# Performance work log

Hardware: AMD Instinct MI355X
Metric: run time of the kernel (lower is better)

## Reference

```python
import jax, jax.numpy as jnp
import numpy as np

B, S, H = 2, 2048, 1024
NH, HD = 16, 64  # num heads, head dim
EPS = 1e-12

def layernorm(x, g, b):
    mu = jnp.mean(x, axis=-1, keepdims=True)
    var = jnp.mean(jnp.square(x - mu), axis=-1, keepdims=True)
    return (x - mu) / jnp.sqrt(var + EPS) * g + b

def setup_inputs() -> dict:
    key = jax.random.key(0)
    ks = jax.random.split(key, 6)
    sd = 0.02
    return {
        "x": jax.random.normal(ks[0], (B, S, H), jnp.float32),
        "ln1_g": jnp.ones((H,), jnp.float32),
        "ln1_b": jnp.zeros((H,), jnp.float32),
        "w_qkv": jax.random.normal(ks[1], (H, 3 * H), jnp.float32) * sd,
        "b_qkv": jnp.zeros((3 * H,), jnp.float32),
        "w_dense": jax.random.normal(ks[2], (H, H), jnp.float32) * sd,
        "b_dense": jnp.zeros((H,), jnp.float32),
        "ln2_g": jnp.ones((H,), jnp.float32),
        "ln2_b": jnp.zeros((H,), jnp.float32),
        "w_fc1": jax.random.normal(ks[3], (H, 2 * H), jnp.float32) * sd,
        "w_fc2": jax.random.normal(ks[4], (2 * H, H), jnp.float32) * sd,
        "b_fc2": jnp.zeros((H,), jnp.float32),
    }

def reference(x, ln1_g, ln1_b, w_qkv, b_qkv, w_dense, b_dense,
              ln2_g, ln2_b, w_fc1, w_fc2, b_fc2):
    b, s, h = x.shape
    qkv = layernorm(x, ln1_g, ln1_b) @ w_qkv + b_qkv          # (b, s, 3h)
    q, k, v = jnp.split(qkv, 3, axis=-1)
    # (b, s, h) -> (b, nh, s, hd)
    reshape = lambda t: t.reshape(b, s, NH, HD).transpose(0, 2, 1, 3)
    q, k, v = reshape(q), reshape(k), reshape(v)
    scores = jnp.einsum('bhqd,bhkd->bhqk', q, k) / jnp.sqrt(jnp.float32(HD))
    causal = jnp.tril(jnp.ones((s, s), dtype=bool))
    scores = jnp.where(causal, scores, -jnp.inf)
    probs = jax.nn.softmax(scores, axis=-1)
    attn = jnp.einsum('bhqk,bhkd->bhqd', probs, v)            # (b, nh, s, hd)
    attn = attn.transpose(0, 2, 1, 3).reshape(b, s, h)
    out = x + (attn @ w_dense + b_dense)
    m = layernorm(out, ln2_g, ln2_b)
    mlp = jax.nn.gelu(m @ w_fc1, approximate=False) @ w_fc2 + b_fc2
    return out + mlp
```

## Files before the change

### kernel.cpp

```cpp
#include <hip/hip_runtime.h>
#include <hip/hip_bf16.h>

typedef __bf16 bf16x8 __attribute__((ext_vector_type(8)));
typedef float  f32x4  __attribute__((ext_vector_type(4)));

typedef __attribute__((address_space(3))) unsigned int as3_u32;
typedef __attribute__((address_space(1))) unsigned int as1_u32;

__device__ __forceinline__ void gld_lds16(const void* gptr, void* lptr){
  __builtin_amdgcn_global_load_lds((const as1_u32*)gptr, (as3_u32*)lptr, 16, 0, 0);
}

__global__ __launch_bounds__(256) void transpose_all(
    const float* __restrict__ w_qkv, const float* __restrict__ w_dense,
    const float* __restrict__ w_fc1, const float* __restrict__ w_fc2,
    __bf16* __restrict__ oqkv, __bf16* __restrict__ oden,
    __bf16* __restrict__ ofc1, __bf16* __restrict__ ofc2){
  __shared__ float tile[32][33];
  int idx = blockIdx.x;
  const float* in; __bf16* out; int R, C;
  if (idx < 3072){ in = w_qkv;  out = oqkv; R = 1024; C = 3072; }
  else if (idx < 4096){ idx -= 3072; in = w_dense; out = oden; R = 1024; C = 1024; }
  else if (idx < 6144){ idx -= 4096; in = w_fc1;  out = ofc1; R = 1024; C = 2048; }
  else { idx -= 6144; in = w_fc2;  out = ofc2; R = 2048; C = 1024; }
  const int ntx = C >> 5;
  const int c0 = (idx % ntx)*32, r0 = (idx / ntx)*32;
  const int tx = threadIdx.x, ty = threadIdx.y;
  #pragma unroll
  for (int i=0;i<32;i+=8)
    tile[ty+i][tx] = in[(size_t)(r0+ty+i)*C + c0+tx];
  __syncthreads();
  #pragma unroll
  for (int i=0;i<32;i+=8)
    out[(size_t)(c0+ty+i)*R + r0+tx] = (__bf16)tile[tx][ty+i];
}

__global__ __launch_bounds__(256) void ln_kernel(const float* __restrict__ x, const float* __restrict__ g,
                                                 const float* __restrict__ b, __bf16* __restrict__ out){
  const int row = blockIdx.x, t = threadIdx.x;
  const float4 v = ((const float4*)(x + (size_t)row*1024))[t];
  float s = v.x+v.y+v.z+v.w;
  #pragma unroll
  for (int m=1;m<64;m<<=1) s += __shfl_xor(s, m);
  __shared__ float red[8];
  if ((t&63)==0) red[t>>6] = s;
  __syncthreads();
  const float mu = (red[0]+red[1]+red[2]+red[3]) * (1.f/1024.f);
  const float d0=v.x-mu, d1=v.y-mu, d2=v.z-mu, d3=v.w-mu;
  float sq = d0*d0+d1*d1+d2*d2+d3*d3;
  #pragma unroll
  for (int m=1;m<64;m<<=1) sq += __shfl_xor(sq, m);
  if ((t&63)==0) red[4+(t>>6)] = sq;
  __syncthreads();
  const float var = (red[4]+red[5]+red[6]+red[7]) * (1.f/1024.f);
  const float inv = rsqrtf(var + 1e-12f);
  const float4 gv = ((const float4*)g)[t];
  const float4 bv = ((const float4*)b)[t];
  union { __bf16 h[4]; uint2 u; } pk;
  pk.h[0]=(__bf16)(d0*inv*gv.x+bv.x); pk.h[1]=(__bf16)(d1*inv*gv.y+bv.y);
  pk.h[2]=(__bf16)(d2*inv*gv.z+bv.z); pk.h[3]=(__bf16)(d3*inv*gv.w+bv.w);
  *(uint2*)(out + (size_t)row*1024 + t*4) = pk.u;
}

template<int MODE>
__global__ __launch_bounds__(256) void gemm_bt(
    const __bf16* __restrict__ A, const __bf16* __restrict__ Bt,
    const float* __restrict__ bias,
    __bf16* __restrict__ outB,
    __bf16* __restrict__ qO, __bf16* __restrict__ kO, __bf16* __restrict__ vtO,
    int M, int N, int K)
{
  __shared__ __align__(16) __bf16 As[2][128*32];
  __shared__ __align__(16) __bf16 Bs[2][128*32];
  const int tid = threadIdx.x;
  const int lane = tid & 63, wave = tid >> 6;
  const int wr = wave >> 1, wc = wave & 1;
  const int l15 = lane & 15, lg = lane >> 4;
  const int bm = blockIdx.x, bn = blockIdx.y;
  const __bf16* Ab = A  + (size_t)bm*128*K;
  const __bf16* Bb = Bt + (size_t)bn*128*K;
  f32x4 acc[4][4] = {};
  const int r0 = tid >> 2;
  const int c0 = (tid & 3) * 8;

  auto stage = [&](int kt, int b){
    const int k0 = kt*32;
    char* dA = (char*)&As[b][0] + wave*1024;
    char* dB = (char*)&Bs[b][0] + wave*1024;
    gld_lds16(Ab + (size_t)r0*K      + k0 + c0, dA);
    gld_lds16(Ab + (size_t)(r0+64)*K + k0 + c0, dA + 4096);
    gld_lds16(Bb + (size_t)r0*K      + k0 + c0, dB);
    gld_lds16(Bb + (size_t)(r0+64)*K + k0 + c0, dB + 4096);
  };

  const int nk = K >> 5;
  stage(0, 0);
  __syncthreads();
  for (int kt = 0; kt < nk; ++kt){
    const int b = kt & 1;
    if (kt+1 < nk) stage(kt+1, b^1);
    bf16x8 af[4], bfv[4];
    #pragma unroll
    for (int i=0;i<4;++i){
      af[i]  = *(const bf16x8*)&As[b][(wr*64 + i*16 + l15)*32 + lg*8];
      bfv[i] = *(const bf16x8*)&Bs[b][(wc*64 + i*16 + l15)*32 + lg*8];
    }
    #pragma unroll
    for (int i=0;i<4;++i)
      #pragma unroll
      for (int j=0;j<4;++j)
        acc[i][j] = __builtin_amdgcn_mfma_f32_16x16x32_bf16(af[i], bfv[j], acc[i][j], 0,0,0);
    __syncthreads();
  }
  #pragma unroll
  for (int i=0;i<4;++i){
    #pragma unroll
    for (int j=0;j<4;++j){
      const int col = bn*128 + wc*64 + j*16 + l15;
      float bv;
      if constexpr (MODE==2) bv = 0.f; else bv = bias[col];
      #pragma unroll
      for (int r=0;r<4;++r){
        const int row = bm*128 + wr*64 + i*16 + lg*4 + r;
        float v = acc[i][j][r] + bv;
        if constexpr (MODE==0){
          const int b_ = row >> 11, s_ = row & 2047;
          if (col < 1024){
            const int h = col>>6, d = col&63;
            qO[((size_t)(b_*16+h)*2048 + s_)*64 + d] = (__bf16)v;
          } else if (col < 2048){
            const int h = (col-1024)>>6, d = (col-1024)&63;
            kO[((size_t)(b_*16+h)*2048 + s_)*64 + d] = (__bf16)v;
          } else {
            const int h = (col-2048)>>6, d = (col-2048)&63;
            vtO[((size_t)(b_*16+h)*64 + d)*2048 + s_] = (__bf16)v;
          }
        } else {
          const float gl = 0.5f*v*(1.f + erff(v*0.70710678118f));
          outB[(size_t)row*N + col] = (__bf16)gl;
        }
      }
    }
  }
}

__global__ __launch_bounds__(256) void gemm_bt64(
    const __bf16* __restrict__ A, const __bf16* __restrict__ Bt,
    const float* __restrict__ bias, const float* __restrict__ resid,
    float* __restrict__ outF, int M, int N, int K)
{
  __shared__ __align__(16) __bf16 As[2][128*32];
  __shared__ __align__(16) __bf16 Bs[2][64*32];
  const int tid = threadIdx.x;
  const int lane = tid & 63, wave = tid >> 6;
  const int l15 = lane & 15, lg = lane >> 4;
  const int bm = blockIdx.x, bn = blockIdx.y;
  const __bf16* Ab = A  + (size_t)bm*128*K;
  const __bf16* Bb = Bt + (size_t)bn*64*K;
  f32x4 acc[2][4] = {};
  const int r0 = tid >> 2;
  const int c0 = (tid & 3) * 8;

  auto stage = [&](int kt, int b){
    const int k0 = kt*32;
    char* dA = (char*)&As[b][0] + wave*1024;
    char* dB = (char*)&Bs[b][0] + wave*1024;
    gld_lds16(Ab + (size_t)r0*K      + k0 + c0, dA);
    gld_lds16(Ab + (size_t)(r0+64)*K + k0 + c0, dA + 4096);
    gld_lds16(Bb + (size_t)r0*K      + k0 + c0, dB);
  };

  const int nk = K >> 5;
  stage(0, 0);
  __syncthreads();
  for (int kt = 0; kt < nk; ++kt){
    const int b = kt & 1;
    if (kt+1 < nk) stage(kt+1, b^1);
    bf16x8 af[2], bfv[4];
    #pragma unroll
    for (int i=0;i<2;++i)
      af[i]  = *(const bf16x8*)&As[b][(wave*32 + i*16 + l15)*32 + lg*8];
    #pragma unroll
    for (int j=0;j<4;++j)
      bfv[j] = *(const bf16x8*)&Bs[b][(j*16 + l15)*32 + lg*8];
    #pragma unroll
    for (int i=0;i<2;++i)
      #pragma unroll
      for (int j=0;j<4;++j)
        acc[i][j] = __builtin_amdgcn_mfma_f32_16x16x32_bf16(af[i], bfv[j], acc[i][j], 0,0,0);
    __syncthreads();
  }
  #pragma unroll
  for (int i=0;i<2;++i){
    #pragma unroll
    for (int j=0;j<4;++j){
      const int col = bn*64 + j*16 + l15;
      const float bv = bias[col];
      #pragma unroll
      for (int r=0;r<4;++r){
        const int row = bm*128 + wave*32 + i*16 + lg*4 + r;
        outF[(size_t)row*N + col] = acc[i][j][r] + bv + resid[(size_t)row*N + col];
      }
    }
  }
}

__global__ __launch_bounds__(512, 4) void attn_kernel(
    const __bf16* __restrict__ Q, const __bf16* __restrict__ K,
    const __bf16* __restrict__ Vt, __bf16* __restrict__ out)
{
  __shared__ __align__(16) __bf16 Ks[2][128*64];
  __shared__ __align__(16) __bf16 Vs[2][2][64*64];
  __shared__ __align__(16) __bf16 Pl[8][16*64];
  const int tid = threadIdx.x;
  const int lane = tid & 63, wave = tid >> 6;
  const int l15 = lane & 15, lg = lane >> 4;
  const int bh = blockIdx.y;
  const int nqb = (int)gridDim.x;
  const int qblk = (bh & 16) ? (int)blockIdx.x : (nqb - 1 - (int)blockIdx.x);
  const int qb = qblk * 128;
  const int qw = qb + wave*16;
  const __bf16* Qh = Q + (size_t)bh*2048*64;
  const char*  Khc = (const char*)(K  + (size_t)bh*2048*64);
  const char*  Vhc = (const char*)(Vt + (size_t)bh*64*2048);

  bf16x8 qf[2];
  #pragma unroll
  for (int f=0;f<2;++f){
    bf16x8 t8 = *(const bf16x8*)&Qh[(size_t)(qw + l15)*64 + f*32 + lg*8];
    #pragma unroll
    for (int j=0;j<8;++j) t8[j] = (__bf16)((float)t8[j] * 0.125f);
    qf[f] = t8;
  }

  f32x4 oacc[4] = {};
  float mrun = -1e30f, lrun = 0.f;

  const int swz_st = (((lane&7) ^ (lane>>3)) << 4);
  const int rswz = ((l15 & 7) << 4);
  char* Pw = (char*)&Pl[wave][0];

  const int krow = wave*16 + (lane>>3);
  const int kh   = wave & 1;
  const int dgrp = wave >> 1;
  const int vrow = dgrp*16 + (lane>>3);

  const int nst = qblk + 1;

  {
    gld_lds16(Khc + (size_t)krow*128 + swz_st,     (char*)&Ks[0][0] + wave*2048);
    gld_lds16(Khc + (size_t)(krow+8)*128 + swz_st, (char*)&Ks[0][0] + wave*2048 + 1024);
    const char* s = Vhc + kh*128 + swz_st;
    gld_lds16(s + (size_t)vrow*4096,     (char*)&Vs[0][kh][0] + dgrp*2048);
    gld_lds16(s + (size_t)(vrow+8)*4096, (char*)&Vs[0][kh][0] + dgrp*2048 + 1024);
  }
  __syncthreads();

  for (int st = 0; st < nst; ++st){
    const int cur = st & 1;
    const int kv0 = st*128;
    if (st+1 < nst){
      const size_t nkv0 = (size_t)(kv0 + 128);
      gld_lds16(Khc + (nkv0 + krow)*128 + swz_st,     (char*)&Ks[cur^1][0] + wave*2048);
      gld_lds16(Khc + (nkv0 + krow + 8)*128 + swz_st, (char*)&Ks[cur^1][0] + wave*2048 + 1024);
      const char* s = Vhc + nkv0*2 + kh*128 + swz_st;
      gld_lds16(s + (size_t)vrow*4096,     (char*)&Vs[cur^1][kh][0] + dgrp*2048);
      gld_lds16(s + (size_t)(vrow+8)*4096, (char*)&Vs[cur^1][kh][0] + dgrp*2048 + 1024);
    }
    if (kv0 <= qw + 15){
      const char* Kb = (const char*)&Ks[cur][0];
      f32x4 sc[8];
      #pragma unroll
      for (int t=0;t<8;++t) sc[t] = f32x4{0.f,0.f,0.f,0.f};
      #pragma unroll
      for (int t=0;t<8;++t){
        const int row = t*16 + l15;
        bf16x8 k0 = *(const bf16x8*)(Kb + row*128 + ((lg*16)      ^ rswz));
        bf16x8 k1 = *(const bf16x8*)(Kb + row*128 + ((64 + lg*16) ^ rswz));
        sc[t] = __builtin_amdgcn_mfma_f32_16x16x32_bf16(k0, qf[0], sc[t], 0,0,0);
        sc[t] = __builtin_amdgcn_mfma_f32_16x16x32_bf16(k1, qf[1], sc[t], 0,0,0);
      }
      if (kv0 + 127 > qw){
        const int q = qw + l15;
        #pragma unroll
        for (int t=0;t<8;++t)
          #pragma unroll
          for (int r=0;r<4;++r)
            if (kv0 + t*16 + lg*4 + r > q) sc[t][r] = -1e30f;
      }
      f32x4 mm;
      #pragma unroll
      for (int r=0;r<4;++r){
        float a = fmaxf(fmaxf(sc[0][r],sc[1][r]), fmaxf(sc[2][r],sc[3][r]));
        float b = fmaxf(fmaxf(sc[4][r],sc[5][r]), fmaxf(sc[6][r],sc[7][r]));
        mm[r] = fmaxf(a,b);
      }
      float mx = fmaxf(fmaxf(mm[0],mm[1]), fmaxf(mm[2],mm[3]));
      mx = fmaxf(mx, __shfl_xor(mx, 16));
      mx = fmaxf(mx, __shfl_xor(mx, 32));
      if (!__all(mx <= mrun + 8.0f)){
        const float nm = fmaxf(mrun, mx);
        const float co = exp2f((mrun - nm) * 1.44269504f);
        lrun *= co;
        float cor[4];
        #pragma unroll
        for (int r=0;r<4;++r) cor[r] = __shfl(co, lg*4+r);
        #pragma unroll
        for (int c=0;c<4;++c)
          #pragma unroll
          for (int r=0;r<4;++r)
            oacc[c][r] *= cor[r];
        mrun = nm;
      }
      const float mb = mrun * 1.44269504f;
      #pragma unroll
      for (int t=0;t<8;++t)
        #pragma unroll
        for (int r=0;r<4;++r)
          sc[t][r] = exp2f(sc[t][r]*1.44269504f - mb);
      f32x4 ss;
      #pragma unroll
      for (int r=0;r<4;++r){
        float a = (sc[0][r]+sc[1][r]) + (sc[2][r]+sc[3][r]);
        float b = (sc[4][r]+sc[5][r]) + (sc[6][r]+sc[7][r]);
        ss[r] = a + b;
      }
      float rs = (ss[0]+ss[1]) + (ss[2]+ss[3]);
      rs += __shfl_xor(rs, 16);
      rs += __shfl_xor(rs, 32);
      lrun += rs;
      #pragma unroll
      for (int h=0; h<2; ++h){
        #pragma unroll
        for (int t=0;t<4;++t){
          union { __bf16 hh[4]; uint2 u; } pk4;
          pk4.hh[0] = (__bf16)sc[h*4+t][0];
          pk4.hh[1] = (__bf16)sc[h*4+t][1];
          pk4.hh[2] = (__bf16)sc[h*4+t][2];
          pk4.hh[3] = (__bf16)sc[h*4+t][3];
          *(uint2*)(Pw + l15*128 + ((t*32 + lg*8) ^ rswz)) = pk4.u;
        }
        const char* Vb = (const char*)&Vs[cur][h][0];
        #pragma unroll
        for (int f=0;f<2;++f){
          bf16x8 pa = *(const bf16x8*)(Pw + l15*128 + ((f*64 + lg*16) ^ rswz));
          #pragma unroll
          for (int c=0;c<4;++c){
            bf16x8 vf = *(const bf16x8*)(Vb + (c*16+l15)*128 + ((f*64 + lg*16) ^ rswz));
            oacc[c] = __builtin_amdgcn_mfma_f32_16x16x32_bf16(pa, vf, oacc[c], 0,0,0);
          }
        }
      }
    }
    __syncthreads();
  }

  const int b_ = bh >> 4, h_ = bh & 15;
  float lr[4];
  #pragma unroll
  for (int r=0;r<4;++r) lr[r] = __shfl(lrun, lg*4+r);
  #pragma unroll
  for (int c=0;c<4;++c)
    #pragma unroll
    for (int r=0;r<4;++r){
      const int row = qw + lg*4 + r;
      out[((size_t)(b_*2048 + row))*1024 + h_*64 + c*16 + l15] = (__bf16)(oacc[c][r] / lr[r]);
    }
}

extern "C" void kernel_launch(void* const* d_in, const int* in_sizes, int n_in,
                              void* d_out, int out_size, void* d_ws, size_t ws_size,
                              hipStream_t stream) {
  const float* x      = (const float*)d_in[0];
  const float* ln1_g  = (const float*)d_in[1];
  const float* ln1_b  = (const float*)d_in[2];
  const float* w_qkv  = (const float*)d_in[3];
  const float* b_qkv  = (const float*)d_in[4];
  const float* w_dense= (const float*)d_in[5];
  const float* b_dense= (const float*)d_in[6];
  const float* ln2_g  = (const float*)d_in[7];
  const float* ln2_b  = (const float*)d_in[8];
  const float* w_fc1  = (const float*)d_in[9];
  const float* w_fc2  = (const float*)d_in[10];
  const float* b_fc2  = (const float*)d_in[11];

  char* ws = (char*)d_ws;
  __bf16* wqkvT  = (__bf16*)(ws + 0);
  __bf16* wdenT  = (__bf16*)(ws + 6291456);
  __bf16* wfc1T  = (__bf16*)(ws + 8388608);
  __bf16* wfc2T  = (__bf16*)(ws + 12582912);
  __bf16* xn     = (__bf16*)(ws + 16777216);
  __bf16* Qb     = (__bf16*)(ws + 25165824);
  __bf16* Kb     = (__bf16*)(ws + 33554432);
  __bf16* Vtb    = (__bf16*)(ws + 41943040);
  __bf16* attnb  = (__bf16*)(ws + 50331648);
  float*  outf   = (float*) (ws + 58720256);
  __bf16* mb     = (__bf16*)(ws + 75497472);
  __bf16* h1b    = (__bf16*)(ws + 83886080);

  transpose_all<<<8192, dim3(32,8), 0, stream>>>(w_qkv, w_dense, w_fc1, w_fc2,
                                                 wqkvT, wdenT, wfc1T, wfc2T);
  ln_kernel<<<4096, 256, 0, stream>>>(x, ln1_g, ln1_b, xn);
  gemm_bt<0><<<dim3(32,24), 256, 0, stream>>>(xn, wqkvT, b_qkv,
                                              nullptr, Qb, Kb, Vtb, 4096, 3072, 1024);
  attn_kernel<<<dim3(16,32), 512, 0, stream>>>(Qb, Kb, Vtb, attnb);
  gemm_bt64<<<dim3(32,16), 256, 0, stream>>>(attnb, wdenT, b_dense, x,
                                             outf, 4096, 1024, 1024);
  ln_kernel<<<4096, 256, 0, stream>>>(outf, ln2_g, ln2_b, mb);
  gemm_bt<2><<<dim3(32,16), 256, 0, stream>>>(mb, wfc1T, nullptr,
                                              h1b, nullptr, nullptr, nullptr, 4096, 2048, 1024);
  gemm_bt64<<<dim3(32,16), 256, 0, stream>>>(h1b, wfc2T, b_fc2, outf,
                                             (float*)d_out, 4096, 1024, 2048);
}
```

Baseline: 192.4 us.

## Process 32 query rows per wave in attention, halving waves per block

The attention kernel now runs 4 waves per block instead of 8. Each wave handles two 16-row query tiles, so every K and V fragment read from LDS feeds two MFMAs instead of one. This is meant to cut LDS read traffic and per-wave softmax overhead for each unit of MFMA work. In exchange it raises register pressure (two sets of scores and accumulators), lowers occupancy, and drops the per-wave causal skip of fully masked tiles, which adds wasted compute on diagonal blocks.

```diff
diff --git a/kernel.cpp b/kernel.cpp
--- a/kernel.cpp
+++ b/kernel.cpp
@@ -205,13 +205,13 @@
   }
 }
 
-__global__ __launch_bounds__(512, 4) void attn_kernel(
+__global__ __launch_bounds__(256, 2) void attn_kernel(
     const __bf16* __restrict__ Q, const __bf16* __restrict__ K,
     const __bf16* __restrict__ Vt, __bf16* __restrict__ out)
 {
   __shared__ __align__(16) __bf16 Ks[2][128*64];
   __shared__ __align__(16) __bf16 Vs[2][2][64*64];
-  __shared__ __align__(16) __bf16 Pl[8][16*64];
+  __shared__ __align__(16) __bf16 Pl[4][32*64];
   const int tid = threadIdx.x;
   const int lane = tid & 63, wave = tid >> 6;
   const int l15 = lane & 15, lg = lane >> 4;
@@ -219,40 +219,41 @@
   const int nqb = (int)gridDim.x;
   const int qblk = (bh & 16) ? (int)blockIdx.x : (nqb - 1 - (int)blockIdx.x);
   const int qb = qblk * 128;
-  const int qw = qb + wave*16;
+  const int qw = qb + wave*32;
   const __bf16* Qh = Q + (size_t)bh*2048*64;
   const char*  Khc = (const char*)(K  + (size_t)bh*2048*64);
   const char*  Vhc = (const char*)(Vt + (size_t)bh*64*2048);
 
-  bf16x8 qf[2];
-  #pragma unroll
-  for (int f=0;f<2;++f){
-    bf16x8 t8 = *(const bf16x8*)&Qh[(size_t)(qw + l15)*64 + f*32 + lg*8];
-    #pragma unroll
-    for (int j=0;j<8;++j) t8[j] = (__bf16)((float)t8[j] * 0.125f);
-    qf[f] = t8;
-  }
-
-  f32x4 oacc[4] = {};
-  float mrun = -1e30f, lrun = 0.f;
+  bf16x8 qf[2][2];
+  #pragma unroll
+  for (int qi=0;qi<2;++qi)
+    #pragma unroll
+    for (int f=0;f<2;++f){
+      bf16x8 t8 = *(const bf16x8*)&Qh[(size_t)(qw + qi*16 + l15)*64 + f*32 + lg*8];
+      #pragma unroll
+      for (int j=0;j<8;++j) t8[j] = (__bf16)((float)t8[j] * 0.125f);
+      qf[qi][f] = t8;
+    }
+
+  f32x4 oacc[2][4] = {};
+  float mrun[2] = {-1e30f, -1e30f}, lrun[2] = {0.f, 0.f};
 
   const int swz_st = (((lane&7) ^ (lane>>3)) << 4);
   const int rswz = ((l15 & 7) << 4);
   char* Pw = (char*)&Pl[wave][0];
 
-  const int krow = wave*16 + (lane>>3);
+  const int krow = wave*32 + (lane>>3);
   const int kh   = wave & 1;
   const int dgrp = wave >> 1;
-  const int vrow = dgrp*16 + (lane>>3);
+  const int vrow = dgrp*32 + (lane>>3);
 
   const int nst = qblk + 1;
 
-  {
-    gld_lds16(Khc + (size_t)krow*128 + swz_st,     (char*)&Ks[0][0] + wave*2048);
-    gld_lds16(Khc + (size_t)(krow+8)*128 + swz_st, (char*)&Ks[0][0] + wave*2048 + 1024);
-    const char* s = Vhc + kh*128 + swz_st;
-    gld_lds16(s + (size_t)vrow*4096,     (char*)&Vs[0][kh][0] + dgrp*2048);
-    gld_lds16(s + (size_t)(vrow+8)*4096, (char*)&Vs[0][kh][0] + dgrp*2048 + 1024);
+  #pragma unroll
+  for (int i=0;i<4;++i){
+    gld_lds16(Khc + (size_t)(krow + i*8)*128 + swz_st, (char*)&Ks[0][0] + wave*4096 + i*1024);
+    gld_lds16(Vhc + (size_t)(vrow + i*8)*4096 + kh*128 + swz_st,
+              (char*)&Vs[0][kh][0] + dgrp*4096 + i*1024);
   }
   __syncthreads();
 
@@ -261,93 +262,119 @@
     const int kv0 = st*128;
     if (st+1 < nst){
       const size_t nkv0 = (size_t)(kv0 + 128);
-      gld_lds16(Khc + (nkv0 + krow)*128 + swz_st,     (char*)&Ks[cur^1][0] + wave*2048);
-      gld_lds16(Khc + (nkv0 + krow + 8)*128 + swz_st, (char*)&Ks[cur^1][0] + wave*2048 + 1024);
-      const char* s = Vhc + nkv0*2 + kh*128 + swz_st;
-      gld_lds16(s + (size_t)vrow*4096,     (char*)&Vs[cur^1][kh][0] + dgrp*2048);
-      gld_lds16(s + (size_t)(vrow+8)*4096, (char*)&Vs[cur^1][kh][0] + dgrp*2048 + 1024);
-    }
-    if (kv0 <= qw + 15){
+      #pragma unroll
+      for (int i=0;i<4;++i){
+        gld_lds16(Khc + (nkv0 + krow + i*8)*128 + swz_st,
+                  (char*)&Ks[cur^1][0] + wave*4096 + i*1024);
+        gld_lds16(Vhc + (size_t)(vrow + i*8)*4096 + nkv0*2 + kh*128 + swz_st,
+                  (char*)&Vs[cur^1][kh][0] + dgrp*4096 + i*1024);
+      }
+    }
+    {
       const char* Kb = (const char*)&Ks[cur][0];
-      f32x4 sc[8];
-      #pragma unroll
-      for (int t=0;t<8;++t) sc[t] = f32x4{0.f,0.f,0.f,0.f};
+      f32x4 sc[2][8];
+      #pragma unroll
+      for (int qi=0;qi<2;++qi)
+        #pragma unroll
+        for (int t=0;t<8;++t) sc[qi][t] = f32x4{0.f,0.f,0.f,0.f};
       #pragma unroll
       for (int t=0;t<8;++t){
         const int row = t*16 + l15;
         bf16x8 k0 = *(const bf16x8*)(Kb + row*128 + ((lg*16)      ^ rswz));
         bf16x8 k1 = *(const bf16x8*)(Kb + row*128 + ((64 + lg*16) ^ rswz));
-        sc[t] = __builtin_amdgcn_mfma_f32_16x16x32_bf16(k0, qf[0], sc[t], 0,0,0);
-        sc[t] = __builtin_amdgcn_mfma_f32_16x16x32_bf16(k1, qf[1], sc[t], 0,0,0);
+        sc[0][t] = __builtin_amdgcn_mfma_f32_16x16x32_bf16(k0, qf[0][0], sc[0][t], 0,0,0);
+        sc[0][t] = __builtin_amdgcn_mfma_f32_16x16x32_bf16(k1, qf[0][1], sc[0][t], 0,0,0);
+        sc[1][t] = __builtin_amdgcn_mfma_f32_16x16x32_bf16(k0, qf[1][0], sc[1][t], 0,0,0);
+        sc[1][t] = __builtin_amdgcn_mfma_f32_16x16x32_bf16(k1, qf[1][1], sc[1][t], 0,0,0);
       }
       if (kv0 + 127 > qw){
-        const int q = qw + l15;
+        #pragma unroll
+        for (int qi=0;qi<2;++qi){
+          const int q = qw + qi*16 + l15;
+          #pragma unroll
+          for (int t=0;t<8;++t)
+            #pragma unroll
+            for (int r=0;r<4;++r)
+              if (kv0 + t*16 + lg*4 + r > q) sc[qi][t][r] = -1e30f;
+        }
+      }
+      float mx[2];
+      #pragma unroll
+      for (int qi=0;qi<2;++qi){
+        f32x4 mm;
+        #pragma unroll
+        for (int r=0;r<4;++r){
+          float a = fmaxf(fmaxf(sc[qi][0][r],sc[qi][1][r]), fmaxf(sc[qi][2][r],sc[qi][3][r]));
+          float b = fmaxf(fmaxf(sc[qi][4][r],sc[qi][5][r]), fmaxf(sc[qi][6][r],sc[qi][7][r]));
+          mm[r] = fmaxf(a,b);
+        }
+        float m = fmaxf(fmaxf(mm[0],mm[1]), fmaxf(mm[2],mm[3]));
+        m = fmaxf(m, __shfl_xor(m, 16));
+        m = fmaxf(m, __shfl_xor(m, 32));
+        mx[qi] = m;
+      }
+      if (!__all((mx[0] <= mrun[0] + 8.0f) && (mx[1] <= mrun[1] + 8.0f))){
+        #pragma unroll
+        for (int qi=0;qi<2;++qi){
+          const float nm = fmaxf(mrun[qi], mx[qi]);
+          const float co = exp2f((mrun[qi] - nm) * 1.44269504f);
+          lrun[qi] *= co;
+          float cor[4];
+          #pragma unroll
+          for (int r=0;r<4;++r) cor[r] = __shfl(co, lg*4+r);
+          #pragma unroll
+          for (int c=0;c<4;++c)
+            #pragma unroll
+            for (int r=0;r<4;++r)
+              oacc[qi][c][r] *= cor[r];
+          mrun[qi] = nm;
+        }
+      }
+      #pragma unroll
+      for (int qi=0;qi<2;++qi){
+        const float mb = mrun[qi] * 1.44269504f;
         #pragma unroll
         for (int t=0;t<8;++t)
           #pragma unroll
           for (int r=0;r<4;++r)
-            if (kv0 + t*16 + lg*4 + r > q) sc[t][r] = -1e30f;
-      }
-      f32x4 mm;
-      #pragma unroll
-      for (int r=0;r<4;++r){
-        float a = fmaxf(fmaxf(sc[0][r],sc[1][r]), fmaxf(sc[2][r],sc[3][r]));
-        float b = fmaxf(fmaxf(sc[4][r],sc[5][r]), fmaxf(sc[6][r],sc[7][r]));
-        mm[r] = fmaxf(a,b);
-      }
-      float mx = fmaxf(fmaxf(mm[0],mm[1]), fmaxf(mm[2],mm[3]));
-      mx = fmaxf(mx, __shfl_xor(mx, 16));
-      mx = fmaxf(mx, __shfl_xor(mx, 32));
-      if (!__all(mx <= mrun + 8.0f)){
-        const float nm = fmaxf(mrun, mx);
-        const float co = exp2f((mrun - nm) * 1.44269504f);
-        lrun *= co;
-        float cor[4];
-        #pragma unroll
-        for (int r=0;r<4;++r) cor[r] = __shfl(co, lg*4+r);
-        #pragma unroll
-        for (int c=0;c<4;++c)
-          #pragma unroll
-          for (int r=0;r<4;++r)
-            oacc[c][r] *= cor[r];
-        mrun = nm;
-      }
-      const float mb = mrun * 1.44269504f;
-      #pragma unroll
-      for (int t=0;t<8;++t)
-        #pragma unroll
-        for (int r=0;r<4;++r)
-          sc[t][r] = exp2f(sc[t][r]*1.44269504f - mb);
-      f32x4 ss;
-      #pragma unroll
-      for (int r=0;r<4;++r){
-        float a = (sc[0][r]+sc[1][r]) + (sc[2][r]+sc[3][r]);
-        float b = (sc[4][r]+sc[5][r]) + (sc[6][r]+sc[7][r]);
-        ss[r] = a + b;
-      }
-      float rs = (ss[0]+ss[1]) + (ss[2]+ss[3]);
-      rs += __shfl_xor(rs, 16);
-      rs += __shfl_xor(rs, 32);
-      lrun += rs;
+            sc[qi][t][r] = exp2f(sc[qi][t][r]*1.44269504f - mb);
+        f32x4 ss;
+        #pragma unroll
+        for (int r=0;r<4;++r){
+          float a = (sc[qi][0][r]+sc[qi][1][r]) + (sc[qi][2][r]+sc[qi][3][r]);
+          float b = (sc[qi][4][r]+sc[qi][5][r]) + (sc[qi][6][r]+sc[qi][7][r]);
+          ss[r] = a + b;
+        }
+        float rs = (ss[0]+ss[1]) + (ss[2]+ss[3]);
+        rs += __shfl_xor(rs, 16);
+        rs += __shfl_xor(rs, 32);
+        lrun[qi] += rs;
+      }
       #pragma unroll
       for (int h=0; h<2; ++h){
         #pragma unroll
-        for (int t=0;t<4;++t){
-          union { __bf16 hh[4]; uint2 u; } pk4;
-          pk4.hh[0] = (__bf16)sc[h*4+t][0];
-          pk4.hh[1] = (__bf16)sc[h*4+t][1];
-          pk4.hh[2] = (__bf16)sc[h*4+t][2];
-          pk4.hh[3] = (__bf16)sc[h*4+t][3];
-          *(uint2*)(Pw + l15*128 + ((t*32 + lg*8) ^ rswz)) = pk4.u;
+        for (int qi=0;qi<2;++qi){
+          char* Pq = Pw + qi*2048;
+          #pragma unroll
+          for (int t=0;t<4;++t){
+            union { __bf16 hh[4]; uint2 u; } pk4;
+            pk4.hh[0] = (__bf16)sc[qi][h*4+t][0];
+            pk4.hh[1] = (__bf16)sc[qi][h*4+t][1];
+            pk4.hh[2] = (__bf16)sc[qi][h*4+t][2];
+            pk4.hh[3] = (__bf16)sc[qi][h*4+t][3];
+            *(uint2*)(Pq + l15*128 + ((t*32 + lg*8) ^ rswz)) = pk4.u;
+          }
         }
         const char* Vb = (const char*)&Vs[cur][h][0];
         #pragma unroll
         for (int f=0;f<2;++f){
-          bf16x8 pa = *(const bf16x8*)(Pw + l15*128 + ((f*64 + lg*16) ^ rswz));
+          bf16x8 pa0 = *(const bf16x8*)(Pw +        l15*128 + ((f*64 + lg*16) ^ rswz));
+          bf16x8 pa1 = *(const bf16x8*)(Pw + 2048 + l15*128 + ((f*64 + lg*16) ^ rswz));
           #pragma unroll
           for (int c=0;c<4;++c){
             bf16x8 vf = *(const bf16x8*)(Vb + (c*16+l15)*128 + ((f*64 + lg*16) ^ rswz));
-            oacc[c] = __builtin_amdgcn_mfma_f32_16x16x32_bf16(pa, vf, oacc[c], 0,0,0);
+            oacc[0][c] = __builtin_amdgcn_mfma_f32_16x16x32_bf16(pa0, vf, oacc[0][c], 0,0,0);
+            oacc[1][c] = __builtin_amdgcn_mfma_f32_16x16x32_bf16(pa1, vf, oacc[1][c], 0,0,0);
           }
         }
       }
@@ -356,16 +383,19 @@
   }
 
   const int b_ = bh >> 4, h_ = bh & 15;
-  float lr[4];
-  #pragma unroll
-  for (int r=0;r<4;++r) lr[r] = __shfl(lrun, lg*4+r);
-  #pragma unroll
-  for (int c=0;c<4;++c)
-    #pragma unroll
-    for (int r=0;r<4;++r){
-      const int row = qw + lg*4 + r;
-      out[((size_t)(b_*2048 + row))*1024 + h_*64 + c*16 + l15] = (__bf16)(oacc[c][r] / lr[r]);
-    }
+  #pragma unroll
+  for (int qi=0;qi<2;++qi){
+    float lr[4];
+    #pragma unroll
+    for (int r=0;r<4;++r) lr[r] = __shfl(lrun[qi], lg*4+r);
+    #pragma unroll
+    for (int c=0;c<4;++c)
+      #pragma unroll
+      for (int r=0;r<4;++r){
+        const int row = qw + qi*16 + lg*4 + r;
+        out[((size_t)(b_*2048 + row))*1024 + h_*64 + c*16 + l15] = (__bf16)(oacc[qi][c][r] / lr[r]);
+      }
+  }
 }
 
 extern "C" void kernel_launch(void* const* d_in, const int* in_sizes, int n_in,
@@ -403,7 +433,7 @@
   ln_kernel<<<4096, 256, 0, stream>>>(x, ln1_g, ln1_b, xn);
   gemm_bt<0><<<dim3(32,24), 256, 0, stream>>>(xn, wqkvT, b_qkv,
                                               nullptr, Qb, Kb, Vtb, 4096, 3072, 1024);
-  attn_kernel<<<dim3(16,32), 512, 0, stream>>>(Qb, Kb, Vtb, attnb);
+  attn_kernel<<<dim3(16,32), 256, 0, stream>>>(Qb, Kb, Vtb, attnb);
   gemm_bt64<<<dim3(32,16), 256, 0, stream>>>(attnb, wdenT, b_dense, x,
                                              outf, 4096, 1024, 1024);
   ln_kernel<<<4096, 256, 0, stream>>>(outf, ln2_g, ln2_b, mb);
```

Measured after the change: 198.2 us. 3.0% more time.

## Fuse weight transpose with first layernorm; stage V-transpose stores through LDS

Applied to the files above, without the earlier changes.

Merges the weight transpose/convert kernel and the first layernorm into one launch, with block index choosing the role. This saves a kernel launch and lets the two independent jobs overlap. In the QKV GEMM epilogue, the V part is written transposed into LDS with an XOR swizzle and then stored as coalesced 16-byte rows, replacing scattered 2-byte strided global writes. This adds extra barriers and LDS traffic in the epilogue.

```diff
diff --git a/kernel.cpp b/kernel.cpp
--- a/kernel.cpp
+++ b/kernel.cpp
@@ -11,28 +11,57 @@
   __builtin_amdgcn_global_load_lds((const as1_u32*)gptr, (as3_u32*)lptr, 16, 0, 0);
 }
 
-__global__ __launch_bounds__(256) void transpose_all(
+__global__ __launch_bounds__(256) void prep_kernel(
     const float* __restrict__ w_qkv, const float* __restrict__ w_dense,
     const float* __restrict__ w_fc1, const float* __restrict__ w_fc2,
     __bf16* __restrict__ oqkv, __bf16* __restrict__ oden,
-    __bf16* __restrict__ ofc1, __bf16* __restrict__ ofc2){
+    __bf16* __restrict__ ofc1, __bf16* __restrict__ ofc2,
+    const float* __restrict__ x, const float* __restrict__ g,
+    const float* __restrict__ b, __bf16* __restrict__ ln_out){
   __shared__ float tile[32][33];
+  const int tid = threadIdx.x;
   int idx = blockIdx.x;
-  const float* in; __bf16* out; int R, C;
-  if (idx < 3072){ in = w_qkv;  out = oqkv; R = 1024; C = 3072; }
-  else if (idx < 4096){ idx -= 3072; in = w_dense; out = oden; R = 1024; C = 1024; }
-  else if (idx < 6144){ idx -= 4096; in = w_fc1;  out = ofc1; R = 1024; C = 2048; }
-  else { idx -= 6144; in = w_fc2;  out = ofc2; R = 2048; C = 1024; }
-  const int ntx = C >> 5;
-  const int c0 = (idx % ntx)*32, r0 = (idx / ntx)*32;
-  const int tx = threadIdx.x, ty = threadIdx.y;
-  #pragma unroll
-  for (int i=0;i<32;i+=8)
-    tile[ty+i][tx] = in[(size_t)(r0+ty+i)*C + c0+tx];
-  __syncthreads();
-  #pragma unroll
-  for (int i=0;i<32;i+=8)
-    out[(size_t)(c0+ty+i)*R + r0+tx] = (__bf16)tile[tx][ty+i];
+  if (idx < 8192){
+    const float* in; __bf16* out; int R, C;
+    if (idx < 3072){ in = w_qkv;  out = oqkv; R = 1024; C = 3072; }
+    else if (idx < 4096){ idx -= 3072; in = w_dense; out = oden; R = 1024; C = 1024; }
+    else if (idx < 6144){ idx -= 4096; in = w_fc1;  out = ofc1; R = 1024; C = 2048; }
+    else { idx -= 6144; in = w_fc2;  out = ofc2; R = 2048; C = 1024; }
+    const int ntx = C >> 5;
+    const int c0 = (idx % ntx)*32, r0 = (idx / ntx)*32;
+    const int tx = tid & 31, ty = tid >> 5;
+    #pragma unroll
+    for (int i=0;i<32;i+=8)
+      tile[ty+i][tx] = in[(size_t)(r0+ty+i)*C + c0+tx];
+    __syncthreads();
+    #pragma unroll
+    for (int i=0;i<32;i+=8)
+      out[(size_t)(c0+ty+i)*R + r0+tx] = (__bf16)tile[tx][ty+i];
+  } else {
+    const int row = idx - 8192;
+    float* red = &tile[0][0];
+    const float4 v = ((const float4*)(x + (size_t)row*1024))[tid];
+    float s = v.x+v.y+v.z+v.w;
+    #pragma unroll
+    for (int m=1;m<64;m<<=1) s += __shfl_xor(s, m);
+    if ((tid&63)==0) red[tid>>6] = s;
+    __syncthreads();
+    const float mu = (red[0]+red[1]+red[2]+red[3]) * (1.f/1024.f);
+    const float d0=v.x-mu, d1=v.y-mu, d2=v.z-mu, d3=v.w-mu;
+    float sq = d0*d0+d1*d1+d2*d2+d3*d3;
+    #pragma unroll
+    for (int m=1;m<64;m<<=1) sq += __shfl_xor(sq, m);
+    if ((tid&63)==0) red[4+(tid>>6)] = sq;
+    __syncthreads();
+    const float var = (red[4]+red[5]+red[6]+red[7]) * (1.f/1024.f);
+    const float inv = rsqrtf(var + 1e-12f);
+    const float4 gv = ((const float4*)g)[tid];
+    const float4 bv = ((const float4*)b)[tid];
+    union { __bf16 h[4]; uint2 u; } pk;
+    pk.h[0]=(__bf16)(d0*inv*gv.x+bv.x); pk.h[1]=(__bf16)(d1*inv*gv.y+bv.y);
+    pk.h[2]=(__bf16)(d2*inv*gv.z+bv.z); pk.h[3]=(__bf16)(d3*inv*gv.w+bv.w);
+    *(uint2*)(ln_out + (size_t)row*1024 + tid*4) = pk.u;
+  }
 }
 
 __global__ __launch_bounds__(256) void ln_kernel(const float* __restrict__ x, const float* __restrict__ g,
@@ -112,30 +141,74 @@
         acc[i][j] = __builtin_amdgcn_mfma_f32_16x16x32_bf16(af[i], bfv[j], acc[i][j], 0,0,0);
     __syncthreads();
   }
-  #pragma unroll
-  for (int i=0;i<4;++i){
-    #pragma unroll
-    for (int j=0;j<4;++j){
-      const int col = bn*128 + wc*64 + j*16 + l15;
-      float bv;
-      if constexpr (MODE==2) bv = 0.f; else bv = bias[col];
-      #pragma unroll
-      for (int r=0;r<4;++r){
-        const int row = bm*128 + wr*64 + i*16 + lg*4 + r;
-        float v = acc[i][j][r] + bv;
-        if constexpr (MODE==0){
-          const int b_ = row >> 11, s_ = row & 2047;
-          if (col < 1024){
-            const int h = col>>6, d = col&63;
-            qO[((size_t)(b_*16+h)*2048 + s_)*64 + d] = (__bf16)v;
-          } else if (col < 2048){
-            const int h = (col-1024)>>6, d = (col-1024)&63;
-            kO[((size_t)(b_*16+h)*2048 + s_)*64 + d] = (__bf16)v;
-          } else {
-            const int h = (col-2048)>>6, d = (col-2048)&63;
-            vtO[((size_t)(b_*16+h)*64 + d)*2048 + s_] = (__bf16)v;
+
+  if constexpr (MODE==0){
+    if (bn < 16){
+      #pragma unroll
+      for (int i=0;i<4;++i){
+        #pragma unroll
+        for (int j=0;j<4;++j){
+          const int col = bn*128 + wc*64 + j*16 + l15;
+          const float bv = bias[col];
+          #pragma unroll
+          for (int r=0;r<4;++r){
+            const int row = bm*128 + wr*64 + i*16 + lg*4 + r;
+            const float v = acc[i][j][r] + bv;
+            const int b_ = row >> 11, s_ = row & 2047;
+            if (col < 1024){
+              const int h = col>>6, d = col&63;
+              qO[((size_t)(b_*16+h)*2048 + s_)*64 + d] = (__bf16)v;
+            } else {
+              const int h = (col-1024)>>6, d = (col-1024)&63;
+              kO[((size_t)(b_*16+h)*2048 + s_)*64 + d] = (__bf16)v;
+            }
           }
-        } else {
+        }
+      }
+    } else {
+      const int bnp = bn - 16;
+      const int b_  = (bm*128) >> 11;
+      const int s0  = (bm*128) & 2047;
+      char* T = (char*)&As[0][0];
+      #pragma unroll
+      for (int h=0; h<2; ++h){
+        __syncthreads();
+        if (wc == h){
+          #pragma unroll
+          for (int j=0;j<4;++j){
+            const int c = j*16 + l15;
+            const float bv = bias[2048 + bnp*128 + h*64 + c];
+            #pragma unroll
+            for (int i=0;i<4;++i){
+              const int row = wr*64 + i*16 + lg*4;
+              union { __bf16 hh[4]; uint2 u; } p4;
+              #pragma unroll
+              for (int r=0;r<4;++r) p4.hh[r] = (__bf16)(acc[i][j][r] + bv);
+              *(uint2*)(T + ((c*256 + row*2) ^ ((c&7)<<4))) = p4.u;
+            }
+          }
+        }
+        __syncthreads();
+        const int c = tid & 63;
+        const int q = tid >> 6;
+        __bf16* dst = vtO + ((size_t)(b_*16 + bnp*2 + h)*64 + c)*2048 + s0;
+        #pragma unroll
+        for (int it=0; it<4; ++it){
+          const int rr = it*32 + q*8;
+          *(uint4*)(dst + rr) = *(const uint4*)(T + ((c*256 + rr*2) ^ ((c&7)<<4)));
+        }
+      }
+    }
+  } else {
+    #pragma unroll
+    for (int i=0;i<4;++i){
+      #pragma unroll
+      for (int j=0;j<4;++j){
+        const int col = bn*128 + wc*64 + j*16 + l15;
+        #pragma unroll
+        for (int r=0;r<4;++r){
+          const int row = bm*128 + wr*64 + i*16 + lg*4 + r;
+          const float v = acc[i][j][r];
           const float gl = 0.5f*v*(1.f + erff(v*0.70710678118f));
           outB[(size_t)row*N + col] = (__bf16)gl;
         }
@@ -398,9 +471,9 @@
   __bf16* mb     = (__bf16*)(ws + 75497472);
   __bf16* h1b    = (__bf16*)(ws + 83886080);
 
-  transpose_all<<<8192, dim3(32,8), 0, stream>>>(w_qkv, w_dense, w_fc1, w_fc2,
-                                                 wqkvT, wdenT, wfc1T, wfc2T);
-  ln_kernel<<<4096, 256, 0, stream>>>(x, ln1_g, ln1_b, xn);
+  prep_kernel<<<12288, 256, 0, stream>>>(w_qkv, w_dense, w_fc1, w_fc2,
+                                         wqkvT, wdenT, wfc1T, wfc2T,
+                                         x, ln1_g, ln1_b, xn);
   gemm_bt<0><<<dim3(32,24), 256, 0, stream>>>(xn, wqkvT, b_qkv,
                                               nullptr, Qb, Kb, Vtb, 4096, 3072, 1024);
   attn_kernel<<<dim3(16,32), 512, 0, stream>>>(Qb, Kb, Vtb, attnb);
```

Result: slower. 201.4 us (+4.6%).
